# Kernel tuning notes

Measured on AMD Instinct MI355X. Metric: run time of the kernel, lower is better.

Reference implementation:

```python
import jax, jax.numpy as jnp
import numpy as np

B, T, N, D, H, E = 64, 64, 32, 32, 128, 256


def setup_inputs() -> dict:
    key = jax.random.key(0)
    ks = jax.random.split(key, 20)

    def g(k, shape, scale=0.1):
        return (jax.random.normal(k, shape, dtype=jnp.float32) * scale)

    return {
        "ts_batch": jax.random.normal(ks[0], (B, T, N, D), dtype=jnp.float32),
        "edge_index": jax.random.randint(ks[1], (2, E), 0, N, dtype=jnp.int32),
        # encoder: 2-layer GCN-LSTM, gates packed as [i,f,g,o] -> 4H
        "Wen0": g(ks[2], (D + H, 4 * H)), "ben0": jnp.zeros((4 * H,), jnp.float32),
        "Wen1": g(ks[3], (2 * H, 4 * H)), "ben1": jnp.zeros((4 * H,), jnp.float32),
        # decoder: 2-layer GCN-LSTM
        "Wde0": g(ks[4], (D + H, 4 * H)), "bde0": jnp.zeros((4 * H,), jnp.float32),
        "Wde1": g(ks[5], (2 * H, 4 * H)), "bde1": jnp.zeros((4 * H,), jnp.float32),
        # per-node linears (the nn.ModuleList loops, batched as [N, in, out])
        "Wmu": g(ks[6], (N, H, H)), "bmu": jnp.zeros((N, H), jnp.float32),
        "Wlv": g(ks[7], (N, H, H)), "blv": jnp.zeros((N, H), jnp.float32),
        "Who": g(ks[8], (N, H, D)), "bho": jnp.zeros((N, D), jnp.float32),
        "Wholv": g(ks[9], (N, H, D)), "bholv": jnp.zeros((N, D), jnp.float32),
        # reparametrization noise (torch.randn_like), made explicit for determinism
        "eps": jax.random.normal(ks[10], (B, N, H), dtype=jnp.float32),
    }


def reference(ts_batch, edge_index, Wen0, ben0, Wen1, ben1, Wde0, bde0, Wde1, bde1,
              Wmu, bmu, Wlv, blv, Who, bho, Wholv, bholv, eps):
    n = Wmu.shape[0]
    # GCN normalized adjacency with self-loops: D^{-1/2}(A+I)D^{-1/2}
    A = jnp.zeros((n, n), jnp.float32).at[edge_index[1], edge_index[0]].add(1.0)
    A = A + jnp.eye(n, dtype=jnp.float32)
    dinv = jax.lax.rsqrt(A.sum(axis=1))
    A = dinv[:, None] * A * dinv[None, :]

    def gcn(x, W, b):  # x: [B,N,F] -> [B,N,4H]
        return jnp.einsum('ij,bjf->bif', A, x) @ W + b

    def cell(x, h, c, W, b):
        z = gcn(jnp.concatenate([x, h], axis=-1), W, b)
        i, f, g, o = jnp.split(z, 4, axis=-1)
        c = jax.nn.sigmoid(f) * c + jax.nn.sigmoid(i) * jnp.tanh(g)
        h = jax.nn.sigmoid(o) * jnp.tanh(c)
        return h, c

    def pnl(x, W, b):  # per-node linear, replaces the python loop over ModuleList
        return jnp.einsum('bnh,nho->bno', x, W) + b

    bsz, tlen = ts_batch.shape[0], ts_batch.shape[1]
    hdim = Wen0.shape[1] // 4
    z0 = jnp.zeros((bsz, n, hdim), jnp.float32)

    def enc_step(carry, x_t):
        h0, c0, h1, c1 = carry
        h0, c0 = cell(x_t, h0, c0, Wen0, ben0)
        h1, c1 = cell(h0, h1, c1, Wen1, ben1)
        return (h0, c0, h1, c1), None

    (h0, c0, h1, c1), _ = jax.lax.scan(
        enc_step, (z0, z0, z0, z0), jnp.transpose(ts_batch, (1, 0, 2, 3)))

    mu = pnl(h1, Wmu, bmu)
    logvar = pnl(h1, Wlv, blv)
    zlat = mu + eps * jnp.exp(logvar)  # reparametrize (note: exp(logvar), as in source)

    out_last = pnl(zlat, Who, bho)
    outlv_last = pnl(zlat, Wholv, bholv)

    # decoder initialized from encoder final (pre-reparam) hidden state; runs in
    # reverse time feeding back its own output (inference / no teacher forcing)
    def dec_step(carry, _):
        h0, c0, h1, c1, prev = carry
        h0, c0 = cell(prev, h0, c0, Wde0, bde0)
        h1, c1 = cell(h0, h1, c1, Wde1, bde1)
        out = pnl(h1, Who, bho)
        outlv = pnl(h1, Wholv, bholv)
        return (h0, c0, h1, c1, out), (out, outlv)

    _, (outs, outlvs) = jax.lax.scan(
        dec_step, (h0, c0, h1, c1, out_last), None, length=tlen - 1)

    # outs are for timesteps T-2 .. 0; reverse and append step T-1
    output = jnp.concatenate([outs[::-1], out_last[None]], axis=0)
    output_logvar = jnp.concatenate([outlvs[::-1], outlv_last[None]], axis=0)
    output = jnp.transpose(output, (1, 0, 2, 3))            # [B,T,N,D]
    output_logvar = jnp.transpose(output_logvar, (1, 0, 2, 3))
    return output, zlat, mu, logvar, output_logvar
```

## Files before the change

### kernel.cpp

```cpp
#include <hip/hip_runtime.h>


typedef unsigned short u16;
typedef unsigned int u32;
typedef short bf16x8 __attribute__((ext_vector_type(8)));
typedef float f32x4 __attribute__((ext_vector_type(4)));

#define O_OUT 0
#define O_Z   4194304
#define O_MU  4456448
#define O_LV  4718592
#define O_OLV 4980736

#define WS_ABF  0
#define WS_PEN0 1280
#define WS_PEN1 83200
#define WS_PDE0 214272
#define WS_PDE1 296192
#define WS_PHO  427264
#define WS_PLV  558336
#define WS_H1   689408
#define WS_NEED_BYTES 34408960ull

#define XSTR 936

__device__ __forceinline__ u16 f2b(float f){
  unsigned x = __float_as_uint(f);
  x += 0x7fffu + ((x>>16)&1u);
  return (u16)(x>>16);
}
__device__ __forceinline__ float b2f(u16 u){ return __uint_as_float(((unsigned)u)<<16); }
__device__ __forceinline__ float blo(unsigned u){ return __uint_as_float(u<<16); }
__device__ __forceinline__ float bhi(unsigned u){ return __uint_as_float(u & 0xffff0000u); }

__device__ __forceinline__ float rcp_(float x){ return __builtin_amdgcn_rcpf(x); }
__device__ __forceinline__ float sigm(float x){ return rcp_(1.f + __expf(-x)); }
__device__ __forceinline__ float tanh_(float x){
  float e = __expf(-2.f*fabsf(x));
  float r = (1.f - e) * rcp_(1.f + e);
  return __builtin_copysignf(r, x);
}

__global__ void adj_kernel(const int* __restrict__ ei, u16* __restrict__ ws)
{
  __shared__ float As[1024];
  __shared__ float dinv[32];
  const int tid = threadIdx.x;
  for (int e = tid; e < 1024; e += 256) As[e] = 0.f;
  __syncthreads();
  atomicAdd(&As[ei[256 + tid]*32 + ei[tid]], 1.f);
  __syncthreads();
  if (tid < 32) As[tid*33] += 1.f;
  __syncthreads();
  if (tid < 32){
    float s = 0.f;
    for (int j=0;j<32;++j) s += As[tid*32 + j];
    dinv[tid] = rsqrtf(s);
  }
  __syncthreads();
  for (int e = tid; e < 1280; e += 256){
    int i = e / 40, j = e % 40;
    float v = (j < 32) ? As[i*32 + j]*dinv[i]*dinv[j] : 0.f;
    ws[WS_ABF + e] = f2b(v);
  }
}

__global__ void pack_kernel(const float* __restrict__ Wen0, const float* __restrict__ Wen1,
                            const float* __restrict__ Wde0, const float* __restrict__ Wde1,
                            const float* __restrict__ Who,  const float* __restrict__ Wholv,
                            u16* __restrict__ ws)
{
  int id = blockIdx.x*256 + threadIdx.x;
  if (id < 53248){
    const float* W; int KS, dstoff, lid;
    if (id < 10240){ W = Wen0; KS = 5; dstoff = WS_PEN0; lid = id; }
    else if (id < 26624){ W = Wen1; KS = 8; dstoff = WS_PEN1; lid = id - 10240; }
    else if (id < 36864){ W = Wde0; KS = 5; dstoff = WS_PDE0; lid = id - 26624; }
    else { W = Wde1; KS = 8; dstoff = WS_PDE1; lid = id - 36864; }
    int l = lid & 63, rest = lid >> 6;
    int ks = rest % KS, nt = rest / KS;
    int n  = nt*16 + (l & 15);
    int k0 = ks*32 + (l >> 4)*8;
    u16 tmp[8];
    #pragma unroll
    for (int j=0;j<8;++j) tmp[j] = f2b(W[(k0 + j)*512 + n]);
    uint4 v;
    v.x = (unsigned)tmp[0] | ((unsigned)tmp[1] << 16);
    v.y = (unsigned)tmp[2] | ((unsigned)tmp[3] << 16);
    v.z = (unsigned)tmp[4] | ((unsigned)tmp[5] << 16);
    v.w = (unsigned)tmp[6] | ((unsigned)tmp[7] << 16);
    *(uint4*)&ws[dstoff + lid*8] = v;
  } else {
    int e = id - 53248;
    const float* src = (e < 16384) ? Who : Wholv;
    int dsto = (e < 16384) ? WS_PHO : WS_PLV;
    e &= 16383;
    int n = e >> 9, r = e & 511;
    int d = r >> 4, h0 = (r & 15)*8;
    u16 tmp[8];
    #pragma unroll
    for (int j=0;j<8;++j) tmp[j] = f2b(src[(n*128 + h0 + j)*32 + d]);
    uint4 v;
    v.x = (unsigned)tmp[0] | ((unsigned)tmp[1] << 16);
    v.y = (unsigned)tmp[2] | ((unsigned)tmp[3] << 16);
    v.z = (unsigned)tmp[4] | ((unsigned)tmp[5] << 16);
    v.w = (unsigned)tmp[6] | ((unsigned)tmp[7] << 16);
    *(uint4*)&ws[dsto + (n*4096 + d*128 + h0)] = v;
  }
}

template<int KS, int N0>
__device__ __forceinline__ void run_cell(
    const u16* __restrict__ PW, const float* bias4,
    u16* XN, u16* yt,
    const bf16x8 afr0, const bf16x8 afr1,
    f32x4 (&cst)[2], int kb0, int kb1, int hwrite,
    int l15, int lq, int wave)
{
  const bf16x8* PW8 = (const bf16x8*)PW;
  const int lane = lq*16 + l15;
  bf16x8 bw[KS][4];
  #pragma unroll
  for (int ks=0; ks<KS; ++ks){
    #pragma unroll
    for (int g=0; g<4; ++g)
      bw[ks][g] = PW8[((g*8 + wave)*KS + ks)*64 + lane];
  }
  f32x4 acc[2][4];
  #pragma unroll
  for (int mt=0;mt<2;++mt)
    #pragma unroll
    for (int g=0;g<4;++g){ f32x4 z = {0.f,0.f,0.f,0.f}; acc[mt][g] = z; }
  #pragma unroll
  for (int ks=0; ks<KS; ++ks){
    const int off = (ks < N0) ? (kb0 + ks*32) : (kb1 + (ks - N0)*32);
    bf16x8 a0 = *(const bf16x8*)&XN[l15*XSTR + off + lq*8];
    bf16x8 a1 = *(const bf16x8*)&XN[(16 + l15)*XSTR + off + lq*8];
    #pragma unroll
    for (int g=0; g<4; ++g){
      acc[0][g] = __builtin_amdgcn_mfma_f32_16x16x32_bf16(a0, bw[ks][g], acc[0][g], 0, 0, 0);
      acc[1][g] = __builtin_amdgcn_mfma_f32_16x16x32_bf16(a1, bw[ks][g], acc[1][g], 0, 0, 0);
    }
  }
  f32x4 acc2[2][4];
  u32* yt32 = (u32*)yt;
  #pragma unroll
  for (int hh=0; hh<2; ++hh){
    #pragma unroll
    for (int g2=0; g2<2; ++g2){
      const int g = hh*2 + g2;
      #pragma unroll
      for (int mt=0; mt<2; ++mt){
        u32 lo = (u32)f2b(acc[mt][g][0]) | ((u32)f2b(acc[mt][g][1]) << 16);
        u32 hi = (u32)f2b(acc[mt][g][2]) | ((u32)f2b(acc[mt][g][3]) << 16);
        const int base = (g2*16 + l15)*20 + mt*8 + lq*2;
        yt32[base]     = lo;
        yt32[base + 1] = hi;
      }
    }
    #pragma unroll
    for (int g2=0; g2<2; ++g2){
      const int g = hh*2 + g2;
      bf16x8 bfr = *(const bf16x8*)&yt[(g2*16 + l15)*40 + lq*8];
      f32x4 vb = {bias4[g], bias4[g], bias4[g], bias4[g]};
      acc2[0][g] = __builtin_amdgcn_mfma_f32_16x16x32_bf16(afr0, bfr, vb, 0, 0, 0);
      acc2[1][g] = __builtin_amdgcn_mfma_f32_16x16x32_bf16(afr1, bfr, vb, 0, 0, 0);
    }
  }
  const int col = wave*16 + l15;
  #pragma unroll
  for (int mt=0;mt<2;++mt){
    #pragma unroll
    for (int q=0;q<4;++q){
      float iv = sigm(acc2[mt][0][q]);
      float fv = sigm(acc2[mt][1][q]);
      float gv = tanh_(acc2[mt][2][q]);
      float ov = sigm(acc2[mt][3][q]);
      float c  = fv*cst[mt][q] + iv*gv;
      cst[mt][q] = c;
      float h  = ov*tanh_(c);
      XN[(mt*16 + lq*4 + q)*XSTR + hwrite + col] = f2b(h);
    }
  }
}

template<bool SAVE>
__global__ __launch_bounds__(512, 2) void lstm_main(
  const float* __restrict__ ts,
  const float* __restrict__ ben0, const float* __restrict__ ben1,
  const float* __restrict__ bde0, const float* __restrict__ bde1,
  const float* __restrict__ Wmu, const float* __restrict__ bmu,
  const float* __restrict__ Wlv, const float* __restrict__ blv,
  const float* __restrict__ bho, const float* __restrict__ bholv,
  const float* __restrict__ Wholv,
  const float* __restrict__ eps,
  const u16* __restrict__ ws, u16* __restrict__ wsH1,
  float* __restrict__ dout)
{
  __shared__ __align__(16) u16 XN[32*XSTR];
  __shared__ __align__(16) u16 Abf[32*40];
  __shared__ __align__(16) u16 Ytr[8*32*40];
  float* zl = (float*)Ytr;

  const int tid  = threadIdx.x;
  const int lane = tid & 63, wave = tid >> 6;
  const int l15  = lane & 15, lq = lane >> 4;
  const int b    = blockIdx.x;
  u16* yt = Ytr + wave*(32*40);

  for (int e = tid; e < 1280;     e += 512) Abf[e] = ws[WS_ABF + e];
  for (int e = tid; e < 32*XSTR;  e += 512) XN[e] = 0;
  f32x4 c0[2], c1[2];
  {
    f32x4 zz = {0.f,0.f,0.f,0.f};
    c0[0]=c0[1]=c1[0]=c1[1]=zz;
  }
  float biE0[4], biE1[4], biD0[4], biD1[4];
  const int colg = wave*16 + l15;
  #pragma unroll
  for (int g=0; g<4; ++g){
    biE0[g] = ben0[g*128+colg];
    biE1[g] = ben1[g*128+colg];
    biD0[g] = bde0[g*128+colg];
    biD1[g] = bde1[g*128+colg];
  }
  const u16* whoT = ws + WS_PHO;
  const u16* wlvT = ws + WS_PLV;
  __syncthreads();
  const bf16x8 afr0 = *(const bf16x8*)&Abf[l15*40 + lq*8];
  const bf16x8 afr1 = *(const bf16x8*)&Abf[(16 + l15)*40 + lq*8];
  {
    const float* xp = ts + (size_t)(b*64)*1024;
    for (int e = tid; e < 1024; e += 512)
      XN[(e >> 5)*XSTR + (e & 31)] = f2b(xp[e]);
  }
  __syncthreads();

  for (int t=0; t<64; ++t){
    const int ph = t & 1;
    run_cell<5,1>(ws+WS_PEN0, biE0, XN, yt, afr0, afr1, c0,
                  0, 32 + 128*ph, 32 + 128*(1-ph), l15, lq, wave);
    __syncthreads();
    if (t < 63){
      const float* xp = ts + (size_t)(b*64 + t + 1)*1024;
      for (int e = tid; e < 1024; e += 512)
        XN[(e >> 5)*XSTR + (e & 31)] = f2b(xp[e]);
    }
    run_cell<8,4>(ws+WS_PEN1, biE1, XN, yt, afr0, afr1, c1,
                  32 + 128*(1-ph), 288 + 128*ph, 288 + 128*(1-ph), l15, lq, wave);
    __syncthreads();
  }

  for (int k=0;k<8;++k){
    int idx = tid + k*512;
    int n = idx >> 7, o = idx & 127;
    float am = bmu[idx];
    float al = blv[idx];
    for (int h=0; h<128; ++h){
      float hv = b2f(XN[n*XSTR + 288 + h]);
      am += hv * Wmu[(n*128 + h)*128 + o];
      al += hv * Wlv[(n*128 + h)*128 + o];
    }
    float zv = am + eps[b*4096 + idx] * __expf(al);
    zl[idx] = zv;
    dout[O_MU + b*4096 + idx] = am;
    dout[O_LV + b*4096 + idx] = al;
    dout[O_Z  + b*4096 + idx] = zv;
  }
  __syncthreads();
  #pragma unroll
  for (int k=0;k<2;++k){
    int idx = tid + k*512;
    int n = idx >> 5, d = idx & 31;
    float a  = bho[idx];
    float a2 = bholv[idx];
    const u16* wp = whoT + (idx << 7);
    for (int h=0; h<128; ++h){
      float hv = zl[n*128 + h];
      a  += hv * b2f(wp[h]);
      a2 += hv * Wholv[(n*128+h)*32 + d];
    }
    dout[O_OUT + (size_t)(b*64 + 63)*1024 + idx] = a;
    dout[O_OLV + (size_t)(b*64 + 63)*1024 + idx] = a2;
    XN[n*XSTR + d] = f2b(a);
  }
  __syncthreads();

  for (int s=0; s<63; ++s){
    const int pg = s & 1;
    run_cell<5,1>(ws+WS_PDE0, biD0, XN, yt, afr0, afr1, c0,
                  0, 32 + 128*pg, 32 + 128*(1-pg), l15, lq, wave);
    __syncthreads();
    run_cell<8,4>(ws+WS_PDE1, biD1, XN, yt, afr0, afr1, c1,
                  32 + 128*(1-pg), 288 + 128*pg, 288 + 128*(1-pg), l15, lq, wave);
    __syncthreads();
    const int h1b = 288 + 128*(1-pg);
    if (SAVE){
      u16* dst = wsH1 + (size_t)(b*63 + s)*4096;
      for (int k=0;k<8;++k){
        int idx = tid + k*512;
        dst[idx] = XN[(idx >> 7)*XSTR + h1b + (idx & 127)];
      }
    }
    const int tt = 62 - s;
    #pragma unroll
    for (int k=0;k<2;++k){
      int idx = tid + k*512;
      int n = idx >> 5, d = idx & 31;
      float a = bho[idx];
      const u16* wp = whoT + (idx << 7);
      if (SAVE){
        #pragma unroll 4
        for (int h=0; h<128; h+=8){
          uint4 hv = *(const uint4*)&XN[n*XSTR + h1b + h];
          uint4 wv = *(const uint4*)&wp[h];
          a += blo(hv.x)*blo(wv.x) + bhi(hv.x)*bhi(wv.x);
          a += blo(hv.y)*blo(wv.y) + bhi(hv.y)*bhi(wv.y);
          a += blo(hv.z)*blo(wv.z) + bhi(hv.z)*bhi(wv.z);
          a += blo(hv.w)*blo(wv.w) + bhi(hv.w)*bhi(wv.w);
        }
      } else {
        float a2 = bholv[idx];
        const u16* wp2 = wlvT + (idx << 7);
        #pragma unroll 4
        for (int h=0; h<128; h+=8){
          uint4 hv = *(const uint4*)&XN[n*XSTR + h1b + h];
          uint4 wv = *(const uint4*)&wp[h];
          uint4 w2 = *(const uint4*)&wp2[h];
          float s0=blo(hv.x), s1=bhi(hv.x), s2=blo(hv.y), s3=bhi(hv.y);
          float s4=blo(hv.z), s5=bhi(hv.z), s6=blo(hv.w), s7=bhi(hv.w);
          a  += s0*blo(wv.x) + s1*bhi(wv.x) + s2*blo(wv.y) + s3*bhi(wv.y)
              + s4*blo(wv.z) + s5*bhi(wv.z) + s6*blo(wv.w) + s7*bhi(wv.w);
          a2 += s0*blo(w2.x) + s1*bhi(w2.x) + s2*blo(w2.y) + s3*bhi(w2.y)
              + s4*blo(w2.z) + s5*bhi(w2.z) + s6*blo(w2.w) + s7*bhi(w2.w);
        }
        dout[O_OLV + (size_t)(b*64 + tt)*1024 + idx] = a2;
      }
      dout[O_OUT + (size_t)(b*64 + tt)*1024 + idx] = a;
      XN[n*XSTR + d] = f2b(a);
    }
    __syncthreads();
  }
}

__global__ __launch_bounds__(256) void outlv_kernel(
    const u16* __restrict__ wsH1, const u16* __restrict__ ws,
    const float* __restrict__ bholv, float* __restrict__ dout)
{
  const int n = blockIdx.x, t = blockIdx.y, tid = threadIdx.x;
  __shared__ __align__(16) u16 Ls[64*128];
  const int s = 62 - t;
  for (int e = tid; e < 8192; e += 256){
    int b = e >> 7;
    Ls[e] = wsH1[(size_t)(b*63 + s)*4096 + n*128 + (e & 127)];
  }
  __syncthreads();
  const int d = tid & 31, bq = tid >> 5;
  const u16* wp2 = ws + WS_PLV + ((n*32 + d) << 7);
  const float bias = bholv[n*32 + d];
  for (int b = bq; b < 64; b += 8){
    float acc = bias;
    #pragma unroll 4
    for (int h = 0; h < 128; h += 8){
      uint4 sv = *(const uint4*)&Ls[b*128 + h];
      uint4 wv = *(const uint4*)&wp2[h];
      acc += blo(sv.x)*blo(wv.x) + bhi(sv.x)*bhi(wv.x);
      acc += blo(sv.y)*blo(wv.y) + bhi(sv.y)*bhi(wv.y);
      acc += blo(sv.z)*blo(wv.z) + bhi(sv.z)*bhi(wv.z);
      acc += blo(sv.w)*blo(wv.w) + bhi(sv.w)*bhi(wv.w);
    }
    dout[O_OLV + (size_t)(b*64 + t)*1024 + n*32 + d] = acc;
  }
}

extern "C" void kernel_launch(void* const* d_in, const int* in_sizes, int n_in,
                              void* d_out, int out_size, void* d_ws, size_t ws_size,
                              hipStream_t stream)
{
  (void)in_sizes; (void)n_in; (void)out_size;
  const float* ts   = (const float*)d_in[0];
  const int*   ei   = (const int*)d_in[1];
  const float* Wen0 = (const float*)d_in[2];
  const float* ben0 = (const float*)d_in[3];
  const float* Wen1 = (const float*)d_in[4];
  const float* ben1 = (const float*)d_in[5];
  const float* Wde0 = (const float*)d_in[6];
  const float* bde0 = (const float*)d_in[7];
  const float* Wde1 = (const float*)d_in[8];
  const float* bde1 = (const float*)d_in[9];
  const float* Wmu  = (const float*)d_in[10];
  const float* bmu  = (const float*)d_in[11];
  const float* Wlv  = (const float*)d_in[12];
  const float* blv  = (const float*)d_in[13];
  const float* Who  = (const float*)d_in[14];
  const float* bho  = (const float*)d_in[15];
  const float* Wholv= (const float*)d_in[16];
  const float* bholv= (const float*)d_in[17];
  const float* eps  = (const float*)d_in[18];
  u16*   ws   = (u16*)d_ws;
  float* dout = (float*)d_out;
  const bool save = ws_size >= WS_NEED_BYTES;

  adj_kernel<<<1, 256, 0, stream>>>(ei, ws);
  pack_kernel<<<336, 256, 0, stream>>>(Wen0, Wen1, Wde0, Wde1, Who, Wholv, ws);
  if (save){
    lstm_main<true><<<64, 512, 0, stream>>>(ts, ben0, ben1, bde0, bde1, Wmu, bmu, Wlv, blv,
        bho, bholv, Wholv, eps, ws, ws + WS_H1, dout);
    outlv_kernel<<<dim3(32,63), 256, 0, stream>>>(ws + WS_H1, ws, bholv, dout);
  } else {
    lstm_main<false><<<64, 512, 0, stream>>>(ts, ben0, ben1, bde0, bde1, Wmu, bmu, Wlv, blv,
        bho, bholv, Wholv, eps, ws, ws, dout);
  }
}
```

Before: 1.870 ms.

## Split LSTM layers across two wave groups and pipeline encoder layers in time

The block grows from 512 to 1024 threads, split into two groups of eight waves. Group 0 runs layer 0 and group 1 runs layer 1. In the encoder, layer 0 at step t runs alongside layer 1 at step t-1, which needs double-buffered x input slots and one barrier per step instead of two. Each group now keeps only its own cell state and bias registers, which lowers register pressure. In the decoder the two groups take turns because output is fed back, so half the waves sit idle during each cell, and the larger block may cost occupancy and register budget.

```diff
diff --git a/kernel.cpp b/kernel.cpp
--- a/kernel.cpp
+++ b/kernel.cpp
@@ -115,7 +115,7 @@
     u16* XN, u16* yt,
     const bf16x8 afr0, const bf16x8 afr1,
     f32x4 (&cst)[2], int kb0, int kb1, int hwrite,
-    int l15, int lq, int wave)
+    int l15, int lq, int w8)
 {
   const bf16x8* PW8 = (const bf16x8*)PW;
   const int lane = lq*16 + l15;
@@ -124,7 +124,7 @@
   for (int ks=0; ks<KS; ++ks){
     #pragma unroll
     for (int g=0; g<4; ++g)
-      bw[ks][g] = PW8[((g*8 + wave)*KS + ks)*64 + lane];
+      bw[ks][g] = PW8[((g*8 + w8)*KS + ks)*64 + lane];
   }
   f32x4 acc[2][4];
   #pragma unroll
@@ -167,7 +167,7 @@
       acc2[1][g] = __builtin_amdgcn_mfma_f32_16x16x32_bf16(afr1, bfr, vb, 0, 0, 0);
     }
   }
-  const int col = wave*16 + l15;
+  const int col = w8*16 + l15;
   #pragma unroll
   for (int mt=0;mt<2;++mt){
     #pragma unroll
@@ -185,7 +185,7 @@
 }
 
 template<bool SAVE>
-__global__ __launch_bounds__(512, 2) void lstm_main(
+__global__ __launch_bounds__(1024, 4) void lstm_main(
   const float* __restrict__ ts,
   const float* __restrict__ ben0, const float* __restrict__ ben1,
   const float* __restrict__ bde0, const float* __restrict__ bde1,
@@ -199,30 +199,27 @@
 {
   __shared__ __align__(16) u16 XN[32*XSTR];
   __shared__ __align__(16) u16 Abf[32*40];
-  __shared__ __align__(16) u16 Ytr[8*32*40];
+  __shared__ __align__(16) u16 Ytr[16*32*40];
   float* zl = (float*)Ytr;
 
   const int tid  = threadIdx.x;
   const int lane = tid & 63, wave = tid >> 6;
+  const int grp  = wave >> 3;
+  const int w8   = wave & 7;
   const int l15  = lane & 15, lq = lane >> 4;
   const int b    = blockIdx.x;
   u16* yt = Ytr + wave*(32*40);
 
-  for (int e = tid; e < 1280;     e += 512) Abf[e] = ws[WS_ABF + e];
-  for (int e = tid; e < 32*XSTR;  e += 512) XN[e] = 0;
-  f32x4 c0[2], c1[2];
-  {
-    f32x4 zz = {0.f,0.f,0.f,0.f};
-    c0[0]=c0[1]=c1[0]=c1[1]=zz;
-  }
-  float biE0[4], biE1[4], biD0[4], biD1[4];
-  const int colg = wave*16 + l15;
+  for (int e = tid; e < 1280;    e += 1024) Abf[e] = ws[WS_ABF + e];
+  for (int e = tid; e < 32*XSTR; e += 1024) XN[e] = 0;
+  f32x4 cst[2];
+  { f32x4 zz = {0.f,0.f,0.f,0.f}; cst[0] = cst[1] = zz; }
+  float biEnc[4], biDec[4];
+  const int colg = w8*16 + l15;
   #pragma unroll
   for (int g=0; g<4; ++g){
-    biE0[g] = ben0[g*128+colg];
-    biE1[g] = ben1[g*128+colg];
-    biD0[g] = bde0[g*128+colg];
-    biD1[g] = bde1[g*128+colg];
+    biEnc[g] = grp ? ben1[g*128+colg] : ben0[g*128+colg];
+    biDec[g] = grp ? bde1[g*128+colg] : bde0[g*128+colg];
   }
   const u16* whoT = ws + WS_PHO;
   const u16* wlvT = ws + WS_PLV;
@@ -231,33 +228,51 @@
   const bf16x8 afr1 = *(const bf16x8*)&Abf[(16 + l15)*40 + lq*8];
   {
     const float* xp = ts + (size_t)(b*64)*1024;
-    for (int e = tid; e < 1024; e += 512)
-      XN[(e >> 5)*XSTR + (e & 31)] = f2b(xp[e]);
-  }
-  __syncthreads();
-
-  for (int t=0; t<64; ++t){
-    const int ph = t & 1;
-    run_cell<5,1>(ws+WS_PEN0, biE0, XN, yt, afr0, afr1, c0,
-                  0, 32 + 128*ph, 32 + 128*(1-ph), l15, lq, wave);
+    XN[(tid >> 5)*XSTR + (tid & 31)] = f2b(xp[tid]);
+  }
+  __syncthreads();
+
+  const u16* PEN0 = ws + WS_PEN0;
+  const u16* PEN1 = ws + WS_PEN1;
+  for (int i=0; i<=64; ++i){
+    if (grp == 0){
+      float xv0 = 0.f, xv1 = 0.f;
+      if (i < 63){
+        const float* xp = ts + (size_t)(b*64 + i + 1)*1024;
+        xv0 = xp[tid]; xv1 = xp[tid + 512];
+      }
+      if (i < 64){
+        const int xb  = (i & 1) ? 544 : 0;
+        const int h0r = 32 + 128*(1 - (i & 1));
+        const int h0w = 32 + 128*(i & 1);
+        run_cell<5,1>(PEN0, biEnc, XN, yt, afr0, afr1, cst,
+                      xb, h0r, h0w, l15, lq, w8);
+      }
+      if (i < 63){
+        const int xb2 = ((i + 1) & 1) ? 544 : 0;
+        XN[(tid >> 5)*XSTR + xb2 + (tid & 31)] = f2b(xv0);
+        XN[((tid + 512) >> 5)*XSTR + xb2 + ((tid + 512) & 31)] = f2b(xv1);
+      }
+    } else {
+      if (i >= 1){
+        const int t   = i - 1;
+        const int h0r = 32  + 128*(t & 1);
+        const int h1r = 288 + 128*(1 - (t & 1));
+        const int h1w = 288 + 128*(t & 1);
+        run_cell<8,4>(PEN1, biEnc, XN, yt, afr0, afr1, cst,
+                      h0r, h1r, h1w, l15, lq, w8);
+      }
+    }
     __syncthreads();
-    if (t < 63){
-      const float* xp = ts + (size_t)(b*64 + t + 1)*1024;
-      for (int e = tid; e < 1024; e += 512)
-        XN[(e >> 5)*XSTR + (e & 31)] = f2b(xp[e]);
-    }
-    run_cell<8,4>(ws+WS_PEN1, biE1, XN, yt, afr0, afr1, c1,
-                  32 + 128*(1-ph), 288 + 128*ph, 288 + 128*(1-ph), l15, lq, wave);
-    __syncthreads();
-  }
-
-  for (int k=0;k<8;++k){
-    int idx = tid + k*512;
+  }
+
+  for (int k=0;k<4;++k){
+    int idx = tid + k*1024;
     int n = idx >> 7, o = idx & 127;
     float am = bmu[idx];
     float al = blv[idx];
     for (int h=0; h<128; ++h){
-      float hv = b2f(XN[n*XSTR + 288 + h]);
+      float hv = b2f(XN[n*XSTR + 416 + h]);
       am += hv * Wmu[(n*128 + h)*128 + o];
       al += hv * Wlv[(n*128 + h)*128 + o];
     }
@@ -268,9 +283,8 @@
     dout[O_Z  + b*4096 + idx] = zv;
   }
   __syncthreads();
-  #pragma unroll
-  for (int k=0;k<2;++k){
-    int idx = tid + k*512;
+  {
+    int idx = tid;
     int n = idx >> 5, d = idx & 31;
     float a  = bho[idx];
     float a2 = bholv[idx];
@@ -286,26 +300,30 @@
   }
   __syncthreads();
 
+  const u16* PDE0 = ws + WS_PDE0;
+  const u16* PDE1 = ws + WS_PDE1;
   for (int s=0; s<63; ++s){
-    const int pg = s & 1;
-    run_cell<5,1>(ws+WS_PDE0, biD0, XN, yt, afr0, afr1, c0,
-                  0, 32 + 128*pg, 32 + 128*(1-pg), l15, lq, wave);
+    const int dg = 1 - (s & 1);
+    if (grp == 0)
+      run_cell<5,1>(PDE0, biDec, XN, yt, afr0, afr1, cst,
+                    0, 32 + 128*dg, 32 + 128*(1-dg), l15, lq, w8);
     __syncthreads();
-    run_cell<8,4>(ws+WS_PDE1, biD1, XN, yt, afr0, afr1, c1,
-                  32 + 128*(1-pg), 288 + 128*pg, 288 + 128*(1-pg), l15, lq, wave);
+    if (grp == 1)
+      run_cell<8,4>(PDE1, biDec, XN, yt, afr0, afr1, cst,
+                    32 + 128*(1-dg), 288 + 128*dg, 288 + 128*(1-dg), l15, lq, w8);
     __syncthreads();
-    const int h1b = 288 + 128*(1-pg);
+    const int h1b = 288 + 128*(1-dg);
     if (SAVE){
       u16* dst = wsH1 + (size_t)(b*63 + s)*4096;
-      for (int k=0;k<8;++k){
-        int idx = tid + k*512;
+      #pragma unroll
+      for (int k=0;k<4;++k){
+        int idx = tid + k*1024;
         dst[idx] = XN[(idx >> 7)*XSTR + h1b + (idx & 127)];
       }
     }
     const int tt = 62 - s;
-    #pragma unroll
-    for (int k=0;k<2;++k){
-      int idx = tid + k*512;
+    {
+      int idx = tid;
       int n = idx >> 5, d = idx & 31;
       float a = bho[idx];
       const u16* wp = whoT + (idx << 7);
@@ -404,11 +422,11 @@
   adj_kernel<<<1, 256, 0, stream>>>(ei, ws);
   pack_kernel<<<336, 256, 0, stream>>>(Wen0, Wen1, Wde0, Wde1, Who, Wholv, ws);
   if (save){
-    lstm_main<true><<<64, 512, 0, stream>>>(ts, ben0, ben1, bde0, bde1, Wmu, bmu, Wlv, blv,
+    lstm_main<true><<<64, 1024, 0, stream>>>(ts, ben0, ben1, bde0, bde1, Wmu, bmu, Wlv, blv,
         bho, bholv, Wholv, eps, ws, ws + WS_H1, dout);
     outlv_kernel<<<dim3(32,63), 256, 0, stream>>>(ws + WS_H1, ws, bholv, dout);
   } else {
-    lstm_main<false><<<64, 512, 0, stream>>>(ts, ben0, ben1, bde0, bde1, Wmu, bmu, Wlv, blv,
+    lstm_main<false><<<64, 1024, 0, stream>>>(ts, ben0, ben1, bde0, bde1, Wmu, bmu, Wlv, blv,
         bho, bholv, Wholv, eps, ws, ws, dout);
   }
 }
```

After: 2.437 ms. 30.3% more time.
